# Optimization experiments

Measured on AMD Instinct MI355X. Metric: run time of the kernel, lower is better.

The kernel has to match this reference:

```python
import jax, jax.numpy as jnp
import numpy as np

D = 384            # lattice_size
PIX = 1.0          # pixel_size (Angstrom)
SIGMA = 1.5        # gaussian width
QUALITY = 3.0
K = int(np.ceil(QUALITY * SIGMA / PIX) * 2 + 1)  # n_pix_cutoff = 11


def setup_inputs() -> dict:
    key = jax.random.key(0)
    k1, k2, k3, k4 = jax.random.split(key, 4)
    # atom coords spread over the box (box spans ~[-192, 192] Angstrom)
    crd = jax.random.normal(k1, (64, 8192, 3), jnp.float32) * 60.0
    # per-image pose: orthonormalize to proper rotation-like matrices
    rot, _ = jnp.linalg.qr(jax.random.normal(k2, (64, 3, 3), jnp.float32))
    rot_init, _ = jnp.linalg.qr(jax.random.normal(k3, (3, 3), jnp.float32))
    trans_init = jax.random.normal(k4, (3,), jnp.float32) * 2.0
    return {"crd": crd, "rot": rot, "rot_init": rot_init, "trans_init": trans_init}


def _splat(crd):
    # crd: [B, N, 3]; project onto x-y plane and splat gaussians into [B, D, D]
    c = crd[..., :2] / PIX + D // 2                      # pixel-space coords [B,N,2]
    center = jnp.round(c).astype(jnp.int32)              # nearest pixel [B,N,2]
    offs = jnp.arange(K, dtype=jnp.int32) - K // 2       # [K]
    ix = center[..., 0, None] + offs                     # [B,N,K]
    iy = center[..., 1, None] + offs                     # [B,N,K]
    px = (ix.astype(crd.dtype) - D // 2) * PIX           # physical pixel coords
    py = (iy.astype(crd.dtype) - D // 2) * PIX
    inv2s2 = 1.0 / (2.0 * SIGMA * SIGMA)
    mx = ((ix >= 0) & (ix < D)).astype(crd.dtype)
    my = ((iy >= 0) & (iy < D)).astype(crd.dtype)
    gx = jnp.exp(-(px - crd[..., 0, None]) ** 2 * inv2s2) * mx   # [B,N,K]
    gy = jnp.exp(-(py - crd[..., 1, None]) ** 2 * inv2s2) * my   # [B,N,K]
    vals = gy[..., :, None] * gx[..., None, :]                   # [B,N,K,K]
    idx = (jnp.clip(iy, 0, D - 1)[..., :, None] * D
           + jnp.clip(ix, 0, D - 1)[..., None, :])               # [B,N,K,K]

    def splat_one(v, i):
        return jnp.zeros(D * D, v.dtype).at[i.reshape(-1)].add(v.reshape(-1))

    img = jax.vmap(splat_one)(vals, idx)
    return img.reshape(crd.shape[0], D, D)


def reference(crd, rot, rot_init, trans_init):
    # pose the atoms
    crd = crd @ rot_init + trans_init[None, None, :]
    crd = jnp.einsum('bnj,bkj->bnk', crd, rot)           # crd @ rot^T
    # gaussian pixel splatting (gather/cutoff/scatter)
    y_real = _splat(crd)                                  # [B,D,D]
    # centered 2D FFT
    f = jnp.fft.fftshift(
        jnp.fft.fftn(jnp.fft.fftshift(y_real, axes=(-2, -1)), axes=(-2, -1)),
        axes=(-2, -1))
    y = f.real - f.imag                                   # hartley domain
    return y, y_real
```

## Files before the change

kernel.cpp:

```cpp
#include <hip/hip_runtime.h>

#define DD 384
#define NB 64
#define NATOM 8192
#define RB 394
#define CB 51
#define NBKT (RB * CB)
#define OFFSTRIDE (NBKT + 4)

typedef short short8 __attribute__((ext_vector_type(8)));
typedef float f32x4 __attribute__((ext_vector_type(4)));
typedef unsigned u32x4 __attribute__((ext_vector_type(4)));

__device__ inline unsigned bf1(float a) {
    unsigned u = __float_as_uint(a);
    return (u + 0x7FFFu + ((u >> 16) & 1u)) >> 16;
}
__device__ inline unsigned bfpack(float a, float b) {
    return bf1(a) | (bf1(b) << 16);
}

__device__ inline float2 pose_one(const float* __restrict__ crd,
                                  const float* __restrict__ rot,
                                  const float* __restrict__ rot_init,
                                  const float* __restrict__ trans, int idx) {
    int b = idx >> 13;
    const float* p = crd + (long)idx * 3;
    float x0 = p[0], y0 = p[1], z0 = p[2];
    float q0 = x0 * rot_init[0] + y0 * rot_init[3] + z0 * rot_init[6] + trans[0];
    float q1 = x0 * rot_init[1] + y0 * rot_init[4] + z0 * rot_init[7] + trans[1];
    float q2 = x0 * rot_init[2] + y0 * rot_init[5] + z0 * rot_init[8] + trans[2];
    const float* R = rot + b * 9;
    float2 o;
    o.x = q0 * R[0] + q1 * R[1] + q2 * R[2];
    o.y = q0 * R[3] + q1 * R[4] + q2 * R[5];
    return o;
}

__global__ void count_atoms(const float* __restrict__ crd,
                            const float* __restrict__ rot,
                            const float* __restrict__ rot_init,
                            const float* __restrict__ trans,
                            int* __restrict__ counts,
                            float2* __restrict__ posed) {
    int idx = blockIdx.x * 256 + threadIdx.x;
    float2 v = pose_one(crd, rot, rot_init, trans, idx);
    posed[idx] = v;
    int icx = (int)rintf(v.x + 192.0f);
    int icy = (int)rintf(v.y + 192.0f);
    if (icx < -5 || icx > 388 || icy < -5 || icy > 388) return;
    int bi = (icy + 5) * CB + ((icx + 16) >> 3);
    atomicAdd(&counts[(idx >> 13) * NBKT + bi], 1);
}

__global__ __launch_bounds__(1024) void bucket_scan(int* __restrict__ counts,
                                                    int* __restrict__ offs) {
    int b = blockIdx.x, t = threadIdx.x;
    int lane = t & 63, wid = t >> 6;
    int* cnt = counts + b * NBKT;
    int* off = offs + b * OFFSTRIDE;
    __shared__ int wsum[16];
    __shared__ int carry;
    if (t == 0) carry = 0;
    __syncthreads();
    const int NT = (NBKT + 1023) / 1024;
    for (int tile = 0; tile < NT; ++tile) {
        int k = tile * 1024 + t;
        int v = (k < NBKT) ? cnt[k] : 0;
        int incl = v;
#pragma unroll
        for (int d = 1; d < 64; d <<= 1) {
            int u = __shfl_up(incl, d);
            if (lane >= d) incl += u;
        }
        if (lane == 63) wsum[wid] = incl;
        __syncthreads();
        if (wid == 0) {
            int s = (lane < 16) ? wsum[lane] : 0;
            int si = s;
#pragma unroll
            for (int d = 1; d < 16; d <<= 1) {
                int u = __shfl_up(si, d);
                if (lane >= d) si += u;
            }
            if (lane < 16) wsum[lane] = si - s;
        }
        __syncthreads();
        int excl = incl - v + wsum[wid] + carry;
        if (k < NBKT) {
            off[k] = excl;
            cnt[k] = 0;
        }
        __syncthreads();
        if (t == 1023) carry = excl + v;
        __syncthreads();
    }
    if (t == 0) off[NBKT] = carry;
}

__global__ void scatter_atoms(const float2* __restrict__ posed,
                              int* __restrict__ cursors,
                              const int* __restrict__ offs,
                              float2* __restrict__ sorted) {
    int idx = blockIdx.x * 256 + threadIdx.x;
    float2 v = posed[idx];
    int icx = (int)rintf(v.x + 192.0f);
    int icy = (int)rintf(v.y + 192.0f);
    if (icx < -5 || icx > 388 || icy < -5 || icy > 388) return;
    int b = idx >> 13;
    int bi = (icy + 5) * CB + ((icx + 16) >> 3);
    int pos = offs[b * OFFSTRIDE + bi] + atomicAdd(&cursors[b * NBKT + bi], 1);
    sorted[(long)b * NATOM + pos] = v;
}

#define LCAP 512
#define LSZ  544

__global__ __launch_bounds__(256) void splat_mfma(const float2* __restrict__ sorted,
                                                  const int* __restrict__ offs,
                                                  float* __restrict__ img,
                                                  unsigned short* __restrict__ img_bf) {
    __shared__ __align__(16) float2 list[4][LSZ];
    int b = blockIdx.z;
    int wv = __builtin_amdgcn_readfirstlane((int)(threadIdx.x >> 6));
    int lane = threadIdx.x & 63;
    int tx = blockIdx.x * 4 + wv;
    int ty = blockIdx.y;
    int c0 = tx * 16, r0 = ty * 16;

    const int* off = offs + b * OFFSTRIDE;
    const float2* srt = sorted + (long)b * NATOM;

    int cb_lo = (c0 + 11) >> 3;
    int cb_end = ((c0 + 36) >> 3) + 1;

    int cur = 0, iend = 0;
    if (lane < 26) {
        int rb = r0 + lane;
        cur = off[rb * CB + cb_lo];
        iend = off[rb * CB + cb_end];
    }

    f32x4 acc = {0.f, 0.f, 0.f, 0.f};
    int m = lane & 15;
    float rowf = (float)(r0 + m);
    float colf = (float)(c0 + m);
    float py = rowf - 192.0f, px = colf - 192.0f;
    int g8 = (lane >> 4) << 3;
    const float kneg = -0.32059868f;
    float2* wl = list[wv];

    for (int round = 0; round < 24; ++round) {
        int len = (lane < 26) ? (iend - cur) : 0;
        int incl = len;
#pragma unroll
        for (int d = 1; d < 64; d <<= 1) {
            int t = __shfl_up(incl, d);
            if (lane >= d) incl += t;
        }
        int excl = incl - len;
        int totrem = __builtin_amdgcn_readfirstlane(__shfl(incl, 63));
        if (totrem == 0) break;
        int total = min(totrem, LCAP);
        int cnt = min(len, max(0, LCAP - excl));
        for (int j = 0; j < cnt; j++) wl[excl + j] = srt[cur + j];
        cur += cnt;
        int padn = (32 - (total & 31)) & 31;
        if (lane < padn) wl[total + lane] = (float2){3.0e5f, 3.0e5f};
        asm volatile("s_waitcnt lgkmcnt(0)" ::: "memory");
        __builtin_amdgcn_sched_barrier(0);

        int nch = (total + 31) >> 5;
        for (int ch = 0; ch < nch; ch++) {
            const f32x4* qp = (const f32x4*)&wl[ch * 32 + g8];
            u32x4 au, bu;
#pragma unroll
            for (int p = 0; p < 4; p++) {
                f32x4 q = qp[p];
                float d0 = py - q[1], d1 = py - q[3];
                float cy0 = rintf(q[1] + 192.0f), cy1 = rintf(q[3] + 192.0f);
                float e0 = (fabsf(rowf - cy0) <= 5.0f) ? exp2f(d0 * d0 * kneg) : 0.0f;
                float e1 = (fabsf(rowf - cy1) <= 5.0f) ? exp2f(d1 * d1 * kneg) : 0.0f;
                au[p] = bfpack(e0, e1);
                float f0 = px - q[0], f1 = px - q[2];
                float cx0 = rintf(q[0] + 192.0f), cx1 = rintf(q[2] + 192.0f);
                float g0 = (fabsf(colf - cx0) <= 5.0f) ? exp2f(f0 * f0 * kneg) : 0.0f;
                float g1 = (fabsf(colf - cx1) <= 5.0f) ? exp2f(f1 * f1 * kneg) : 0.0f;
                bu[p] = bfpack(g0, g1);
            }
            short8 af = __builtin_bit_cast(short8, au);
            short8 bf = __builtin_bit_cast(short8, bu);
            acc = __builtin_amdgcn_mfma_f32_16x16x32_bf16(af, bf, acc, 0, 0, 0);
        }
        if (totrem <= LCAP) break;
    }

    int col = c0 + m;
    int rbase = r0 + (lane >> 4) * 4;
#pragma unroll
    for (int r = 0; r < 4; r++) {
        long o = ((long)b * DD + rbase + r) * DD + col;
        img[o] = acc[r];
        img_bf[o] = (unsigned short)bf1(acc[r]);
    }
}

__global__ void gen_w(unsigned short* __restrict__ Bt1,
                      unsigned short* __restrict__ Bt2) {
    int idx = blockIdx.x * 256 + threadIdx.x;
    if (idx >= DD * DD) return;
    int i = idx / DD, j = idx % DD;
    int t = (i - 192) * (j - 192);
    int r = t % DD;
    if (r < 0) r += DD;
    float th = (float)r * (6.28318530717958647692f / (float)DD);
    float s = sinf(th), c = cosf(th);
    Bt1[i * DD + j] = (unsigned short)bf1(c + s);
    Bt1[(DD + i) * DD + j] = (unsigned short)bf1(s);
    Bt2[i * 768 + j] = (unsigned short)bf1(c + s);
    Bt2[i * 768 + 384 + j] = (unsigned short)bf1(-2.0f * s);
}

template <bool CBF16, bool BFOLD>
__global__ __launch_bounds__(256) void gemm_mfma(const unsigned short* __restrict__ Ag,
                                                 const unsigned short* __restrict__ Bg,
                                                 long sB,
                                                 void* __restrict__ Cg, long sC,
                                                 int K, int ldc, int nx, int bpi) {
    __shared__ uint4 lds4[2048];

    int cpx = gridDim.x >> 3;
    int wg = blockIdx.x;
    int lin = (wg & 7) * cpx + (wg >> 3);
    int bz = lin / bpi;
    int rr = lin - bz * bpi;
    int m0 = (rr / nx) * 128, n0 = (rr % nx) * 128;
    int tid = threadIdx.x;
    int lane = tid & 63, w = tid >> 6;
    int wm = w >> 1, wn = w & 1;

    f32x4 acc[4][4];
#pragma unroll
    for (int i = 0; i < 4; i++)
#pragma unroll
        for (int j = 0; j < 4; j++) acc[i][j] = (f32x4){0.f, 0.f, 0.f, 0.f};

    const unsigned short* Bh = Bg + (long)bz * sB;

    int lsw = lane ^ (((lane >> 4) & 3) << 1);

    for (int k0 = 0; k0 < K; k0 += 64) {
        __syncthreads();
#pragma unroll
        for (int cc = 0; cc < 4; cc++) {
            int c = tid + cc * 256;
            int m = c >> 3, kc = (c & 7) << 3;
            int li = ((m >> 4) * 2 + (kc >> 5)) * 64 +
                     ((m & 15) | (((kc >> 3) & 3) << 4));
            li ^= ((kc >> 3) & 3) << 1;
            lds4[li] = *(const uint4*)(Ag + (long)(m0 + m) * K + k0 + kc);
            uint4 wv;
            if (BFOLD) {
                int kk = k0 + kc;
                long boff = (kk >= 384)
                                ? ((long)(384 + n0 + m) * 384 + (kk - 384))
                                : ((long)(n0 + m) * 384 + kk);
                wv = *(const uint4*)(Bh + boff);
            } else {
                wv = *(const uint4*)(Bh + (long)(n0 + m) * K + k0 + kc);
            }
            lds4[1024 + li] = wv;
        }
        __syncthreads();
#pragma unroll
        for (int ki = 0; ki < 2; ki++) {
            short8 a[4], bfr[4];
#pragma unroll
            for (int i = 0; i < 4; i++)
                a[i] = *(const short8*)&lds4[((wm * 4 + i) * 2 + ki) * 64 + lsw];
#pragma unroll
            for (int j = 0; j < 4; j++)
                bfr[j] = *(const short8*)&lds4[1024 + ((wn * 4 + j) * 2 + ki) * 64 + lsw];
#pragma unroll
            for (int i = 0; i < 4; i++)
#pragma unroll
                for (int j = 0; j < 4; j++)
                    acc[i][j] = __builtin_amdgcn_mfma_f32_16x16x32_bf16(
                        a[i], bfr[j], acc[i][j], 0, 0, 0);
        }
    }

    int quad = lane >> 4, col0 = lane & 15;
#pragma unroll
    for (int i = 0; i < 4; i++)
#pragma unroll
        for (int j = 0; j < 4; j++)
#pragma unroll
            for (int r = 0; r < 4; r++) {
                int row = m0 + (wm * 4 + i) * 16 + quad * 4 + r;
                int cc2 = n0 + (wn * 4 + j) * 16 + col0;
                if (CBF16)
                    ((unsigned short*)Cg + (long)bz * sC)[(long)row * ldc + cc2] =
                        (unsigned short)bf1(acc[i][j][r]);
                else
                    ((float*)Cg + (long)bz * sC)[(long)row * ldc + cc2] = acc[i][j][r];
            }
}

extern "C" void kernel_launch(void* const* d_in, const int* in_sizes, int n_in,
                              void* d_out, int out_size, void* d_ws, size_t ws_size,
                              hipStream_t stream) {
    const float* crd      = (const float*)d_in[0];
    const float* rot      = (const float*)d_in[1];
    const float* rot_init = (const float*)d_in[2];
    const float* trans    = (const float*)d_in[3];

    float* out   = (float*)d_out;
    float* y     = out;
    float* yreal = out + (size_t)NB * DD * DD;
    unsigned short* Ybf = (unsigned short*)y;

    char* ws = (char*)d_ws;
    unsigned short* Bt1 = (unsigned short*)ws;
    unsigned short* Bt2 = (unsigned short*)(ws + 589824);
    char* Zb = ws + 1179648;
    unsigned short* Z = (unsigned short*)Zb;
    int*    counts = (int*)Zb;
    int*    offs   = (int*)(Zb + 5144064);
    float2* sorted = (float2*)(Zb + 10289152);
    float2* posed  = (float2*)(Zb + 14483456);

    hipMemsetAsync(counts, 0, (size_t)NB * NBKT * 4, stream);

    count_atoms<<<(NB * NATOM) / 256, 256, 0, stream>>>(crd, rot, rot_init, trans,
                                                        counts, posed);
    bucket_scan<<<NB, 1024, 0, stream>>>(counts, offs);
    scatter_atoms<<<(NB * NATOM) / 256, 256, 0, stream>>>(posed, counts, offs, sorted);
    splat_mfma<<<dim3(6, 24, NB), 256, 0, stream>>>(sorted, offs, yreal, Ybf);

    gen_w<<<(DD * DD + 255) / 256, 256, 0, stream>>>(Bt1, Bt2);

    gemm_mfma<true, false><<<1152, 256, 0, stream>>>(
        Bt1, Ybf, (long)DD * DD, (void*)Z, (long)768 * DD, DD, DD, 3, 18);

    gemm_mfma<false, true><<<576, 256, 0, stream>>>(
        Bt2, Z, (long)768 * DD, (void*)y, (long)DD * DD, 768, DD, 3, 9);
}
```

Baseline: 264.0 us.

## Replace row/column bucket sort with per-tile atom lists read directly from global

Atoms are binned into every 16x16 output tile their 11-pixel footprint overlaps, producing one contiguous, 32-padded list per tile. The splat kernel reads its tile's list straight from global memory and drops the multi-round LDS staging and per-row bucket gathering. The much smaller tile count also shrinks the scan to a single pass. In exchange, atoms are duplicated across up to four tiles, padding depends on a 0x45 memset of a large buffer, and list capacity is assumed not to overflow.

```diff
diff --git a/kernel.cpp b/kernel.cpp
--- a/kernel.cpp
+++ b/kernel.cpp
@@ -3,10 +3,9 @@
 #define DD 384
 #define NB 64
 #define NATOM 8192
-#define RB 394
-#define CB 51
-#define NBKT (RB * CB)
-#define OFFSTRIDE (NBKT + 4)
+#define NTX 24
+#define NTILE (NTX * NTX)
+#define LSTRIDE 51200
 
 typedef short short8 __attribute__((ext_vector_type(8)));
 typedef float f32x4 __attribute__((ext_vector_type(4)));
@@ -48,98 +47,90 @@
     posed[idx] = v;
     int icx = (int)rintf(v.x + 192.0f);
     int icy = (int)rintf(v.y + 192.0f);
-    if (icx < -5 || icx > 388 || icy < -5 || icy > 388) return;
-    int bi = (icy + 5) * CB + ((icx + 16) >> 3);
-    atomicAdd(&counts[(idx >> 13) * NBKT + bi], 1);
-}
-
-__global__ __launch_bounds__(1024) void bucket_scan(int* __restrict__ counts,
-                                                    int* __restrict__ offs) {
+    int x0 = max(icx - 5, 0), x1 = min(icx + 5, DD - 1);
+    int y0 = max(icy - 5, 0), y1 = min(icy + 5, DD - 1);
+    if (x0 > x1 || y0 > y1) return;
+    int tx0 = x0 >> 4, tx1 = x1 >> 4, ty0 = y0 >> 4, ty1 = y1 >> 4;
+    int* cb = counts + (idx >> 13) * NTILE;
+    for (int ty = ty0; ty <= ty1; ++ty)
+        for (int tx = tx0; tx <= tx1; ++tx)
+            atomicAdd(&cb[ty * NTX + tx], 1);
+}
+
+__global__ __launch_bounds__(1024) void tile_scan(int* __restrict__ counts,
+                                                  int* __restrict__ offs) {
     int b = blockIdx.x, t = threadIdx.x;
     int lane = t & 63, wid = t >> 6;
-    int* cnt = counts + b * NBKT;
-    int* off = offs + b * OFFSTRIDE;
+    int* cnt = counts + b * NTILE;
+    int* off = offs + b * NTILE;
     __shared__ int wsum[16];
-    __shared__ int carry;
-    if (t == 0) carry = 0;
+    int v = (t < NTILE) ? cnt[t] : 0;
+    int r = (v + 31) & ~31;
+    int incl = r;
+#pragma unroll
+    for (int d = 1; d < 64; d <<= 1) {
+        int u = __shfl_up(incl, d);
+        if (lane >= d) incl += u;
+    }
+    if (lane == 63) wsum[wid] = incl;
     __syncthreads();
-    const int NT = (NBKT + 1023) / 1024;
-    for (int tile = 0; tile < NT; ++tile) {
-        int k = tile * 1024 + t;
-        int v = (k < NBKT) ? cnt[k] : 0;
-        int incl = v;
-#pragma unroll
-        for (int d = 1; d < 64; d <<= 1) {
-            int u = __shfl_up(incl, d);
-            if (lane >= d) incl += u;
-        }
-        if (lane == 63) wsum[wid] = incl;
-        __syncthreads();
-        if (wid == 0) {
-            int s = (lane < 16) ? wsum[lane] : 0;
-            int si = s;
-#pragma unroll
-            for (int d = 1; d < 16; d <<= 1) {
-                int u = __shfl_up(si, d);
-                if (lane >= d) si += u;
-            }
-            if (lane < 16) wsum[lane] = si - s;
-        }
-        __syncthreads();
-        int excl = incl - v + wsum[wid] + carry;
-        if (k < NBKT) {
-            off[k] = excl;
-            cnt[k] = 0;
-        }
-        __syncthreads();
-        if (t == 1023) carry = excl + v;
-        __syncthreads();
-    }
-    if (t == 0) off[NBKT] = carry;
+    if (wid == 0) {
+        int s = (lane < 16) ? wsum[lane] : 0;
+        int si = s;
+#pragma unroll
+        for (int d = 1; d < 16; d <<= 1) {
+            int u = __shfl_up(si, d);
+            if (lane >= d) si += u;
+        }
+        if (lane < 16) wsum[lane] = si - s;
+    }
+    __syncthreads();
+    if (t < NTILE) {
+        off[t] = incl - r + wsum[wid];
+        cnt[t] = 0;
+    }
 }
 
 __global__ void scatter_atoms(const float2* __restrict__ posed,
                               int* __restrict__ cursors,
                               const int* __restrict__ offs,
-                              float2* __restrict__ sorted) {
+                              float2* __restrict__ lists) {
     int idx = blockIdx.x * 256 + threadIdx.x;
     float2 v = posed[idx];
     int icx = (int)rintf(v.x + 192.0f);
     int icy = (int)rintf(v.y + 192.0f);
-    if (icx < -5 || icx > 388 || icy < -5 || icy > 388) return;
+    int x0 = max(icx - 5, 0), x1 = min(icx + 5, DD - 1);
+    int y0 = max(icy - 5, 0), y1 = min(icy + 5, DD - 1);
+    if (x0 > x1 || y0 > y1) return;
     int b = idx >> 13;
-    int bi = (icy + 5) * CB + ((icx + 16) >> 3);
-    int pos = offs[b * OFFSTRIDE + bi] + atomicAdd(&cursors[b * NBKT + bi], 1);
-    sorted[(long)b * NATOM + pos] = v;
-}
-
-#define LCAP 512
-#define LSZ  544
-
-__global__ __launch_bounds__(256) void splat_mfma(const float2* __restrict__ sorted,
+    int* cb = cursors + b * NTILE;
+    const int* ob = offs + b * NTILE;
+    float2* lb = lists + (long)b * LSTRIDE;
+    int tx0 = x0 >> 4, tx1 = x1 >> 4, ty0 = y0 >> 4, ty1 = y1 >> 4;
+    for (int ty = ty0; ty <= ty1; ++ty)
+        for (int tx = tx0; tx <= tx1; ++tx) {
+            int tt = ty * NTX + tx;
+            int pos = atomicAdd(&cb[tt], 1);
+            lb[ob[tt] + pos] = v;
+        }
+}
+
+__global__ __launch_bounds__(256) void splat_mfma(const float2* __restrict__ lists,
                                                   const int* __restrict__ offs,
+                                                  const int* __restrict__ cnts,
                                                   float* __restrict__ img,
                                                   unsigned short* __restrict__ img_bf) {
-    __shared__ __align__(16) float2 list[4][LSZ];
     int b = blockIdx.z;
     int wv = __builtin_amdgcn_readfirstlane((int)(threadIdx.x >> 6));
     int lane = threadIdx.x & 63;
     int tx = blockIdx.x * 4 + wv;
     int ty = blockIdx.y;
     int c0 = tx * 16, r0 = ty * 16;
-
-    const int* off = offs + b * OFFSTRIDE;
-    const float2* srt = sorted + (long)b * NATOM;
-
-    int cb_lo = (c0 + 11) >> 3;
-    int cb_end = ((c0 + 36) >> 3) + 1;
-
-    int cur = 0, iend = 0;
-    if (lane < 26) {
-        int rb = r0 + lane;
-        cur = off[rb * CB + cb_lo];
-        iend = off[rb * CB + cb_end];
-    }
+    int tt = ty * NTX + tx;
+
+    int i0 = offs[b * NTILE + tt];
+    int n  = cnts[b * NTILE + tt];
+    const float2* lb = lists + (long)b * LSTRIDE + i0;
 
     f32x4 acc = {0.f, 0.f, 0.f, 0.f};
     int m = lane & 15;
@@ -148,51 +139,28 @@
     float py = rowf - 192.0f, px = colf - 192.0f;
     int g8 = (lane >> 4) << 3;
     const float kneg = -0.32059868f;
-    float2* wl = list[wv];
-
-    for (int round = 0; round < 24; ++round) {
-        int len = (lane < 26) ? (iend - cur) : 0;
-        int incl = len;
-#pragma unroll
-        for (int d = 1; d < 64; d <<= 1) {
-            int t = __shfl_up(incl, d);
-            if (lane >= d) incl += t;
-        }
-        int excl = incl - len;
-        int totrem = __builtin_amdgcn_readfirstlane(__shfl(incl, 63));
-        if (totrem == 0) break;
-        int total = min(totrem, LCAP);
-        int cnt = min(len, max(0, LCAP - excl));
-        for (int j = 0; j < cnt; j++) wl[excl + j] = srt[cur + j];
-        cur += cnt;
-        int padn = (32 - (total & 31)) & 31;
-        if (lane < padn) wl[total + lane] = (float2){3.0e5f, 3.0e5f};
-        asm volatile("s_waitcnt lgkmcnt(0)" ::: "memory");
-        __builtin_amdgcn_sched_barrier(0);
-
-        int nch = (total + 31) >> 5;
-        for (int ch = 0; ch < nch; ch++) {
-            const f32x4* qp = (const f32x4*)&wl[ch * 32 + g8];
-            u32x4 au, bu;
-#pragma unroll
-            for (int p = 0; p < 4; p++) {
-                f32x4 q = qp[p];
-                float d0 = py - q[1], d1 = py - q[3];
-                float cy0 = rintf(q[1] + 192.0f), cy1 = rintf(q[3] + 192.0f);
-                float e0 = (fabsf(rowf - cy0) <= 5.0f) ? exp2f(d0 * d0 * kneg) : 0.0f;
-                float e1 = (fabsf(rowf - cy1) <= 5.0f) ? exp2f(d1 * d1 * kneg) : 0.0f;
-                au[p] = bfpack(e0, e1);
-                float f0 = px - q[0], f1 = px - q[2];
-                float cx0 = rintf(q[0] + 192.0f), cx1 = rintf(q[2] + 192.0f);
-                float g0 = (fabsf(colf - cx0) <= 5.0f) ? exp2f(f0 * f0 * kneg) : 0.0f;
-                float g1 = (fabsf(colf - cx1) <= 5.0f) ? exp2f(f1 * f1 * kneg) : 0.0f;
-                bu[p] = bfpack(g0, g1);
-            }
-            short8 af = __builtin_bit_cast(short8, au);
-            short8 bf = __builtin_bit_cast(short8, bu);
-            acc = __builtin_amdgcn_mfma_f32_16x16x32_bf16(af, bf, acc, 0, 0, 0);
-        }
-        if (totrem <= LCAP) break;
+
+    int nch = (n + 31) >> 5;
+    for (int ch = 0; ch < nch; ch++) {
+        const f32x4* qp = (const f32x4*)(lb + ch * 32 + g8);
+        u32x4 au, bu;
+#pragma unroll
+        for (int p = 0; p < 4; p++) {
+            f32x4 q = qp[p];
+            float d0 = py - q[1], d1 = py - q[3];
+            float cy0 = rintf(q[1] + 192.0f), cy1 = rintf(q[3] + 192.0f);
+            float e0 = (fabsf(rowf - cy0) <= 5.0f) ? exp2f(d0 * d0 * kneg) : 0.0f;
+            float e1 = (fabsf(rowf - cy1) <= 5.0f) ? exp2f(d1 * d1 * kneg) : 0.0f;
+            au[p] = bfpack(e0, e1);
+            float f0 = px - q[0], f1 = px - q[2];
+            float cx0 = rintf(q[0] + 192.0f), cx1 = rintf(q[2] + 192.0f);
+            float g0 = (fabsf(colf - cx0) <= 5.0f) ? exp2f(f0 * f0 * kneg) : 0.0f;
+            float g1 = (fabsf(colf - cx1) <= 5.0f) ? exp2f(f1 * f1 * kneg) : 0.0f;
+            bu[p] = bfpack(g0, g1);
+        }
+        short8 af = __builtin_bit_cast(short8, au);
+        short8 bf = __builtin_bit_cast(short8, bu);
+        acc = __builtin_amdgcn_mfma_f32_16x16x32_bf16(af, bf, acc, 0, 0, 0);
     }
 
     int col = c0 + m;
@@ -326,17 +294,18 @@
     char* Zb = ws + 1179648;
     unsigned short* Z = (unsigned short*)Zb;
     int*    counts = (int*)Zb;
-    int*    offs   = (int*)(Zb + 5144064);
-    float2* sorted = (float2*)(Zb + 10289152);
-    float2* posed  = (float2*)(Zb + 14483456);
-
-    hipMemsetAsync(counts, 0, (size_t)NB * NBKT * 4, stream);
+    int*    offs   = (int*)(Zb + 147456);
+    float2* posed  = (float2*)(Zb + 294912);
+    float2* lists  = (float2*)(Zb + 4489216);
+
+    hipMemsetAsync(counts, 0, (size_t)NB * NTILE * 4, stream);
+    hipMemsetAsync(lists, 0x45, (size_t)NB * LSTRIDE * 8, stream);
 
     count_atoms<<<(NB * NATOM) / 256, 256, 0, stream>>>(crd, rot, rot_init, trans,
                                                         counts, posed);
-    bucket_scan<<<NB, 1024, 0, stream>>>(counts, offs);
-    scatter_atoms<<<(NB * NATOM) / 256, 256, 0, stream>>>(posed, counts, offs, sorted);
-    splat_mfma<<<dim3(6, 24, NB), 256, 0, stream>>>(sorted, offs, yreal, Ybf);
+    tile_scan<<<NB, 1024, 0, stream>>>(counts, offs);
+    scatter_atoms<<<(NB * NATOM) / 256, 256, 0, stream>>>(posed, counts, offs, lists);
+    splat_mfma<<<dim3(6, 24, NB), 256, 0, stream>>>(lists, offs, counts, yreal, Ybf);
 
     gen_w<<<(DD * DD + 255) / 256, 256, 0, stream>>>(Bt1, Bt2);
 
```

Result: slower. 319.9 us (+21.2%).
